# Optimization experiments

Hardware: AMD Instinct MI355X
Metric: run time of the kernel (lower is better)

The kernel has to match this reference:

```python
import jax, jax.numpy as jnp
import numpy as np

SR = 44100  # sample_rate from __init__


def setup_inputs() -> dict:
    key = jax.random.key(0)
    k1, k2 = jax.random.split(key)
    x = jax.random.normal(k1, (64, 2, 131072), dtype=jnp.float32) * 0.1
    t = jax.random.uniform(k2, (64,), dtype=jnp.float32)
    filter_freq = jnp.array([1000.0], dtype=jnp.float32)  # learnable param
    filter_q = jnp.array([0.707], dtype=jnp.float32)      # learnable param
    return {"x": x, "t": t, "filter_freq": filter_freq, "filter_q": filter_q}


def _highpass_biquad(x, filter_freq, filter_q):
    # parameter clamping as in the module's forward
    freq = jnp.clip(filter_freq, 100.0, SR / 2.0 - 1.0)[0]
    q = jnp.clip(filter_q, 0.1, 10.0)[0]
    # torchaudio highpass_biquad coefficients
    w0 = 2.0 * jnp.pi * freq / SR
    cosw = jnp.cos(w0)
    alpha = jnp.sin(w0) / (2.0 * q)
    a0 = 1.0 + alpha
    b0 = ((1.0 + cosw) * 0.5) / a0
    b1 = (-(1.0 + cosw)) / a0
    b2 = b0
    a1 = (-2.0 * cosw) / a0
    a2 = (1.0 - alpha) / a0
    # FIR (feedforward) part, zero initial conditions: fused elementwise
    x1 = jnp.pad(x, ((0, 0), (0, 0), (1, 0)))[..., :-1]
    x2 = jnp.pad(x, ((0, 0), (0, 0), (2, 0)))[..., :-2]
    xf = b0 * x + b1 * x1 + b2 * x2  # [B, C, T]
    # IIR (feedback) 2nd-order recurrence over time, vectorized over (B, C)
    xf_t = jnp.moveaxis(xf, -1, 0)  # [T, B, C]

    def step(carry, u):
        y1, y2 = carry
        y = u - a1 * y1 - a2 * y2
        return (y, y1), y

    zero = jnp.zeros(xf_t.shape[1:], xf_t.dtype)
    _, ys = jax.lax.scan(step, (zero, zero), xf_t)
    y = jnp.moveaxis(ys, 0, -1)  # [B, C, T]
    # torchaudio lfilter default clamp=True
    return jnp.clip(y, -1.0, 1.0)


def reference(x, t, filter_freq, filter_q):
    # t is accepted but unused, matching the original forward signature
    return _highpass_biquad(x, filter_freq, filter_q)
```

## Files before the change

kernel.cpp:

```cpp
#include <hip/hip_runtime.h>
#include <math.h>


constexpr int T_LEN  = 131072;
constexpr int L       = 64;
constexpr int CPB     = 64;
constexpr int SEG     = CPB * L;
constexpr int BLK_PER_SEQ = T_LEN / SEG;
constexpr int NSEQ    = 64 * 2;
constexpr int NBLOCKS = NSEQ * BLK_PER_SEQ;

typedef float fx4 __attribute__((ext_vector_type(4)));

#define AS1(p) ((const __attribute__((address_space(1))) void*)(p))
#define AS3(p) ((__attribute__((address_space(3))) void*)(p))

__global__ __launch_bounds__(64) void hp_kernel(
    const float* __restrict__ x,
    const float* __restrict__ pfreq,
    const float* __restrict__ pq,
    float* __restrict__ out)
{
    __shared__ fx4 lds4[CPB * 16];

    float freq = fminf(fmaxf(pfreq[0], 100.0f), 44100.0f * 0.5f - 1.0f);
    float q    = fminf(fmaxf(pq[0], 0.1f), 10.0f);
    float w0   = 2.0f * (float)M_PI * freq / 44100.0f;
    float cw   = cosf(w0);
    float alpha = sinf(w0) / (2.0f * q);
    float ia0  = 1.0f / (1.0f + alpha);
    const float b0 = (1.0f + cw) * 0.5f * ia0;
    const float b1 = -(1.0f + cw) * ia0;
    const float b2 = b0;
    const float a1 = -2.0f * cw * ia0;
    const float a2 = (1.0f - alpha) * ia0;

    const int b   = blockIdx.x;
    const int seq = b >> 5;
    const int S   = (b & (BLK_PER_SEQ - 1)) * SEG;
    const float* __restrict__ xs = x   + (size_t)seq * T_LEN;
    float*       __restrict__ os = out + (size_t)seq * T_LEN;
    const int tid = threadIdx.x;

    {
        const float* gseg = xs + S;
#pragma unroll
        for (int k = 0; k < 16; ++k) {
            int s = tid + (k << 6);
            int r = s >> 4;
            int g = (r << 4) | ((s & 15) ^ (r & 15));
            __builtin_amdgcn_global_load_lds(AS1(gseg + (g << 2)),
                                             AS3(lds4 + (k << 6)), 16, 0, 0);
        }
    }

    fx4 h[16];
    if (tid == 0 && S > 0) {
        const fx4* gw = (const fx4*)(xs + S - L);
#pragma unroll
        for (int k = 0; k < 16; ++k) h[k] = gw[k];
    }

    __syncthreads();

    float y1 = 0.f, y2 = 0.f, p1 = 0.f, p2 = 0.f;

#define STEP(xv) { \
        float xf_ = fmaf(b2, p2, fmaf(b1, p1, b0 * (xv))); \
        float yv  = fmaf(-a1, y1, fmaf(-a2, y2, xf_)); \
        p2 = p1; p1 = (xv); y2 = y1; y1 = yv; }

    const int cgm = (S >> 6) + tid;
    if (cgm >= 1) {
        if (cgm >= 2) {
            if (tid >= 2) {
                int rr = tid - 2;
                const float* pr = (const float*)(lds4 + ((rr << 4) | (15 ^ (rr & 15))));
                p2 = pr[2]; p1 = pr[3];
            } else {
                const float* w = xs + S + (tid - 1) * L;
                p1 = w[-1]; p2 = w[-2];
            }
        }
        const fx4* rp = lds4 + (((tid - 1) & 63) << 4);
        const int  xr = (tid - 1) & 15;
#pragma unroll
        for (int j4 = 0; j4 < 16; ++j4) {
            fx4 v = (tid == 0) ? h[j4] : rp[j4 ^ xr];
            STEP(v.x); STEP(v.y); STEP(v.z); STEP(v.w);
        }
    }

    {
        fx4* mrow = lds4 + (tid << 4);
        const int xm = tid & 15;
#pragma unroll
        for (int j4 = 0; j4 < 16; ++j4) {
            int idx = j4 ^ xm;
            fx4 v = mrow[idx];
            fx4 o;
            STEP(v.x); o.x = fminf(fmaxf(y1, -1.f), 1.f);
            STEP(v.y); o.y = fminf(fmaxf(y1, -1.f), 1.f);
            STEP(v.z); o.z = fminf(fmaxf(y1, -1.f), 1.f);
            STEP(v.w); o.w = fminf(fmaxf(y1, -1.f), 1.f);
            mrow[idx] = o;
        }
    }
    __syncthreads();

    {
        fx4* ob = (fx4*)(os + S);
#pragma unroll
        for (int k = 0; k < 16; ++k) {
            int f = tid + (k << 6);
            int r = f >> 4;
            ob[f] = lds4[(r << 4) | ((f & 15) ^ (r & 15))];
        }
    }
#undef STEP
}

extern "C" void kernel_launch(void* const* d_in, const int* in_sizes, int n_in,
                              void* d_out, int out_size, void* d_ws, size_t ws_size,
                              hipStream_t stream) {
    const float* x  = (const float*)d_in[0];
    const float* ff = (const float*)d_in[2];
    const float* fq = (const float*)d_in[3];
    float* out = (float*)d_out;
    hp_kernel<<<NBLOCKS, CPB, 0, stream>>>(x, ff, fq, out);
}
```

Baseline: 118.4 us.

## Process four segments per block with double-buffered async LDS prefetch and carried state

Each block now walks four consecutive 4096-sample segments instead of one, using two LDS buffers so the next segment's global-to-LDS loads overlap compute on the current one. For later segments, lane 0 takes the exact filter state from lane 63 of the previous segment through shuffles, so it no longer redoes the 64-sample warm-up. The grid is four times smaller, which cuts per-block setup and warm-up reloads but lowers parallelism. Correctness depends on the hand-written vmcnt waits, the single-wavefront block, and the LDS writes being done before the next load into the same buffer.

New measurement: 120.9 us. +2.1%, slower.

```diff
diff --git a/kernel.cpp b/kernel.cpp
--- a/kernel.cpp
+++ b/kernel.cpp
@@ -3,12 +3,13 @@
 
 
 constexpr int T_LEN  = 131072;
-constexpr int L       = 64;
-constexpr int CPB     = 64;
-constexpr int SEG     = CPB * L;
-constexpr int BLK_PER_SEQ = T_LEN / SEG;
-constexpr int NSEQ    = 64 * 2;
-constexpr int NBLOCKS = NSEQ * BLK_PER_SEQ;
+constexpr int L      = 64;
+constexpr int CPB    = 64;
+constexpr int SEG    = CPB * L;
+constexpr int SPB    = 4;
+constexpr int GRP_PER_SEQ = T_LEN / (SEG * SPB);
+constexpr int NSEQ   = 64 * 2;
+constexpr int NBLOCKS = NSEQ * GRP_PER_SEQ;
 
 typedef float fx4 __attribute__((ext_vector_type(4)));
 
@@ -21,7 +22,7 @@
     const float* __restrict__ pq,
     float* __restrict__ out)
 {
-    __shared__ fx4 lds4[CPB * 16];
+    __shared__ fx4 lds4[2][CPB * 16];
 
     float freq = fminf(fmaxf(pfreq[0], 100.0f), 44100.0f * 0.5f - 1.0f);
     float q    = fminf(fmaxf(pq[0], 0.1f), 10.0f);
@@ -36,85 +37,139 @@
     const float a2 = (1.0f - alpha) * ia0;
 
     const int b   = blockIdx.x;
-    const int seq = b >> 5;
-    const int S   = (b & (BLK_PER_SEQ - 1)) * SEG;
+    const int seq = b >> 3;
+    const int S0  = (b & (GRP_PER_SEQ - 1)) * (SEG * SPB);
     const float* __restrict__ xs = x   + (size_t)seq * T_LEN;
     float*       __restrict__ os = out + (size_t)seq * T_LEN;
     const int tid = threadIdx.x;
 
-    {
-        const float* gseg = xs + S;
-#pragma unroll
-        for (int k = 0; k < 16; ++k) {
-            int s = tid + (k << 6);
-            int r = s >> 4;
-            int g = (r << 4) | ((s & 15) ^ (r & 15));
-            __builtin_amdgcn_global_load_lds(AS1(gseg + (g << 2)),
-                                             AS3(lds4 + (k << 6)), 16, 0, 0);
-        }
+    float hp1 = 0.f, hp2 = 0.f;
+    if (S0 > 0 && tid < 2) {
+        const float* w = xs + S0 + (tid - 1) * L;
+        hp1 = w[-1]; hp2 = w[-2];
     }
-
     fx4 h[16];
-    if (tid == 0 && S > 0) {
-        const fx4* gw = (const fx4*)(xs + S - L);
+    if (S0 > 0 && tid == 0) {
+        const fx4* gw = (const fx4*)(xs + S0 - L);
 #pragma unroll
         for (int k = 0; k < 16; ++k) h[k] = gw[k];
     }
 
-    __syncthreads();
+#pragma unroll
+    for (int k = 0; k < 16; ++k) {
+        int s4 = tid + (k << 6);
+        int r  = s4 >> 4;
+        int g  = (r << 4) | ((s4 & 15) ^ (r & 15));
+        __builtin_amdgcn_global_load_lds(AS1(xs + S0 + (g << 2)),
+                                         AS3(&lds4[0][k << 6]), 16, 0, 0);
+    }
+#pragma unroll
+    for (int k = 0; k < 16; ++k) {
+        int s4 = tid + (k << 6);
+        int r  = s4 >> 4;
+        int g  = (r << 4) | ((s4 & 15) ^ (r & 15));
+        __builtin_amdgcn_global_load_lds(AS1(xs + S0 + SEG + (g << 2)),
+                                         AS3(&lds4[1][k << 6]), 16, 0, 0);
+    }
 
-    float y1 = 0.f, y2 = 0.f, p1 = 0.f, p2 = 0.f;
+    float ny1 = 0.f, ny2 = 0.f, np1 = 0.f, np2 = 0.f;
 
 #define STEP(xv) { \
         float xf_ = fmaf(b2, p2, fmaf(b1, p1, b0 * (xv))); \
         float yv  = fmaf(-a1, y1, fmaf(-a2, y2, xf_)); \
         p2 = p1; p1 = (xv); y2 = y1; y1 = yv; }
 
-    const int cgm = (S >> 6) + tid;
-    if (cgm >= 1) {
-        if (cgm >= 2) {
-            if (tid >= 2) {
-                int rr = tid - 2;
-                const float* pr = (const float*)(lds4 + ((rr << 4) | (15 ^ (rr & 15))));
-                p2 = pr[2]; p1 = pr[3];
-            } else {
-                const float* w = xs + S + (tid - 1) * L;
-                p1 = w[-1]; p2 = w[-2];
+#pragma unroll 1
+    for (int s = 0; s < SPB; ++s) {
+        const int S = S0 + s * SEG;
+        fx4* buf = lds4[s & 1];
+
+        asm volatile("s_waitcnt vmcnt(16) lgkmcnt(0)" ::: "memory");
+        __builtin_amdgcn_sched_barrier(0);
+
+        if (s >= 1 && s + 1 < SPB) {
+            fx4* nb = lds4[(s + 1) & 1];
+            const float* gseg = xs + S + SEG;
+#pragma unroll
+            for (int k = 0; k < 16; ++k) {
+                int s4 = tid + (k << 6);
+                int r  = s4 >> 4;
+                int g  = (r << 4) | ((s4 & 15) ^ (r & 15));
+                __builtin_amdgcn_global_load_lds(AS1(gseg + (g << 2)),
+                                                 AS3(&nb[k << 6]), 16, 0, 0);
             }
         }
-        const fx4* rp = lds4 + (((tid - 1) & 63) << 4);
-        const int  xr = (tid - 1) & 15;
+
+        float y1, y2, p1, p2;
+
+        if (s == 0) {
+            y1 = 0.f; y2 = 0.f; p1 = 0.f; p2 = 0.f;
+            const int cgm = (S0 >> 6) + tid;
+            if (cgm >= 1) {
+                if (cgm >= 2) {
+                    if (tid >= 2) {
+                        int rr = tid - 2;
+                        const float* pr = (const float*)
+                            (buf + ((rr << 4) | (15 ^ (rr & 15))));
+                        p2 = pr[2]; p1 = pr[3];
+                    } else { p1 = hp1; p2 = hp2; }
+                }
+                const fx4* rp = buf + (((tid - 1) & 63) << 4);
+                const int  xr = (tid - 1) & 15;
 #pragma unroll
-        for (int j4 = 0; j4 < 16; ++j4) {
-            fx4 v = (tid == 0) ? h[j4] : rp[j4 ^ xr];
-            STEP(v.x); STEP(v.y); STEP(v.z); STEP(v.w);
+                for (int j4 = 0; j4 < 16; ++j4) {
+                    fx4 v = (tid == 0) ? h[j4] : rp[j4 ^ xr];
+                    STEP(v.x); STEP(v.y); STEP(v.z); STEP(v.w);
+                }
+            }
+        } else {
+            if (tid == 0) {
+                y1 = ny1; y2 = ny2; p1 = np1; p2 = np2;
+            } else {
+                y1 = 0.f; y2 = 0.f;
+                if (tid >= 2) {
+                    int rr = tid - 2;
+                    const float* pr = (const float*)
+                        (buf + ((rr << 4) | (15 ^ (rr & 15))));
+                    p2 = pr[2]; p1 = pr[3];
+                } else { p1 = np1; p2 = np2; }
+                const fx4* rp = buf + ((tid - 1) << 4);
+                const int  xr = (tid - 1) & 15;
+#pragma unroll
+                for (int j4 = 0; j4 < 16; ++j4) {
+                    fx4 v = rp[j4 ^ xr];
+                    STEP(v.x); STEP(v.y); STEP(v.z); STEP(v.w);
+                }
+            }
         }
-    }
 
-    {
-        fx4* mrow = lds4 + (tid << 4);
-        const int xm = tid & 15;
+        {
+            fx4* mrow = buf + (tid << 4);
+            const int xm = tid & 15;
 #pragma unroll
-        for (int j4 = 0; j4 < 16; ++j4) {
-            int idx = j4 ^ xm;
-            fx4 v = mrow[idx];
-            fx4 o;
-            STEP(v.x); o.x = fminf(fmaxf(y1, -1.f), 1.f);
-            STEP(v.y); o.y = fminf(fmaxf(y1, -1.f), 1.f);
-            STEP(v.z); o.z = fminf(fmaxf(y1, -1.f), 1.f);
-            STEP(v.w); o.w = fminf(fmaxf(y1, -1.f), 1.f);
-            mrow[idx] = o;
+            for (int j4 = 0; j4 < 16; ++j4) {
+                int idx = j4 ^ xm;
+                fx4 v = mrow[idx];
+                fx4 o;
+                STEP(v.x); o.x = fminf(fmaxf(y1, -1.f), 1.f);
+                STEP(v.y); o.y = fminf(fmaxf(y1, -1.f), 1.f);
+                STEP(v.z); o.z = fminf(fmaxf(y1, -1.f), 1.f);
+                STEP(v.w); o.w = fminf(fmaxf(y1, -1.f), 1.f);
+                mrow[idx] = o;
+            }
         }
-    }
-    __syncthreads();
 
-    {
-        fx4* ob = (fx4*)(os + S);
+        ny1 = __shfl(y1, 63); ny2 = __shfl(y2, 63);
+        np1 = __shfl(p1, 63); np2 = __shfl(p2, 63);
+
+        {
+            fx4* ob = (fx4*)(os + S);
 #pragma unroll
-        for (int k = 0; k < 16; ++k) {
-            int f = tid + (k << 6);
-            int r = f >> 4;
-            ob[f] = lds4[(r << 4) | ((f & 15) ^ (r & 15))];
+            for (int k = 0; k < 16; ++k) {
+                int f = tid + (k << 6);
+                int r = f >> 4;
+                ob[f] = buf[(r << 4) | ((f & 15) ^ (r & 15))];
+            }
         }
     }
 #undef STEP
```
